# Kernel optimization log

Measured on AMD Instinct MI355X. Metric: run time of the kernel, lower is better.

The kernel has to match this reference:

```python
import jax, jax.numpy as jnp
import numpy as np

N, E, G = 50000, 600000, 256
IN_C, EMB, HID, OUT = 64, 128, 128, 36


def _glorot(key, fan_in, fan_out):
    lim = np.sqrt(6.0 / (fan_in + fan_out)).astype(np.float32)
    return jax.random.uniform(key, (fan_in, fan_out), jnp.float32, -lim, lim)


def setup_inputs() -> dict:
    key = jax.random.key(0)
    ks = jax.random.split(key, 12)
    x = jax.random.normal(ks[0], (N, IN_C), jnp.float32)
    edge_index = jax.random.randint(ks[1], (2, E), 0, N, jnp.int64)
    edge_attr = jax.random.uniform(ks[2], (E,), jnp.float32)
    # deterministic sorted batch assignment -> every graph id 0..G-1 is nonempty
    batch = ((jnp.arange(N, dtype=jnp.int64) * G) // N).astype(jnp.int64)
    rho = jax.random.uniform(ks[3], (G,), jnp.float32)
    return {
        "x": x,
        "edge_attr": edge_attr,
        "rho": rho,
        "conv0_w": _glorot(ks[4], IN_C, EMB),
        "conv0_b": jnp.zeros((EMB,), jnp.float32),
        "conv1_w": _glorot(ks[5], EMB, EMB),
        "conv1_b": jnp.zeros((EMB,), jnp.float32),
        "mlp0_w": _glorot(ks[6], 2 * EMB + 1, HID),
        "mlp0_b": jnp.zeros((HID,), jnp.float32),
        "mlp1_w": _glorot(ks[7], HID, HID),
        "mlp1_b": jnp.zeros((HID,), jnp.float32),
        "out_w": _glorot(ks[8], HID, OUT),
        "out_b": jnp.zeros((OUT,), jnp.float32),
        "edge_index": edge_index,
        "batch": batch,
    }


def _gcn_conv(h, row, col, w, W, b):
    # PyG GCNConv: self-loops already appended in (row, col, w).
    deg = jax.ops.segment_sum(w, col, num_segments=N)  # in-degree by edge weight
    dis = jnp.where(deg > 0, jax.lax.rsqrt(jnp.maximum(deg, 1e-30)), 0.0)
    norm = dis[row] * w * dis[col]                     # [E+N]
    h = h @ W                                          # [N, out]
    msg = norm[:, None] * h[row]                       # gather + scale
    return jax.ops.segment_sum(msg, col, num_segments=N) + b


def reference(x, edge_attr, rho, conv0_w, conv0_b, conv1_w, conv1_b,
              mlp0_w, mlp0_b, mlp1_w, mlp1_b, out_w, out_b,
              edge_index, batch):
    # add self-loops with weight 1
    loops = jnp.arange(N, dtype=edge_index.dtype)
    row = jnp.concatenate([edge_index[0], loops])
    col = jnp.concatenate([edge_index[1], loops])
    w = jnp.concatenate([edge_attr, jnp.ones((N,), edge_attr.dtype)])

    h = jax.nn.relu(_gcn_conv(x, row, col, w, conv0_w, conv0_b))
    h = jax.nn.relu(_gcn_conv(h, row, col, w, conv1_w, conv1_b))

    gmp = jax.ops.segment_max(h, batch, num_segments=G)             # [G, EMB]
    cnt = jax.ops.segment_sum(jnp.ones((N,), h.dtype), batch, num_segments=G)
    gap = jax.ops.segment_sum(h, batch, num_segments=G) / cnt[:, None]
    hg = jnp.concatenate([gmp, gap, rho[:, None]], axis=1)          # [G, 2*EMB+1]

    hg = jax.nn.relu(hg @ mlp0_w + mlp0_b)
    hg = jax.nn.relu(hg @ mlp1_w + mlp1_b)
    return hg @ out_w + out_b
```

## Files before the change

### kernel.cpp

```cpp
#include <hip/hip_runtime.h>
#include <hip/hip_fp16.h>
#include <math.h>

using half8 = __attribute__((ext_vector_type(8))) _Float16;
using f32x4 = __attribute__((ext_vector_type(4))) float;

#define CAP 64


__device__ __forceinline__ float wdec(unsigned int v) {
    __half h;
    *reinterpret_cast<unsigned short*>(&h) = (unsigned short)(v >> 16);
    return __half2float(h);
}

__device__ __forceinline__ unsigned int wenc(int src, float w) {
    __half h = __float2half(w);
    return (unsigned int)src |
           ((unsigned int)(*reinterpret_cast<unsigned short*>(&h)) << 16);
}

__device__ __forceinline__ float4 ld_half4(const __half* p) {
    int2 raw = *reinterpret_cast<const int2*>(p);
    __half2 a = *reinterpret_cast<__half2*>(&raw.x);
    __half2 b = *reinterpret_cast<__half2*>(&raw.y);
    return make_float4(__low2float(a), __high2float(a), __low2float(b), __high2float(b));
}

__device__ __forceinline__ void st_half4(__half* p, float4 v) {
    __half2 a = __floats2half2_rn(v.x, v.y);
    __half2 b = __floats2half2_rn(v.z, v.w);
    int2 raw;
    raw.x = *reinterpret_cast<int*>(&a);
    raw.y = *reinterpret_cast<int*>(&b);
    *reinterpret_cast<int2*>(p) = raw;
}


__global__ void k_setup(const float* __restrict__ w0, __half* __restrict__ wt0,
                        const float* __restrict__ w1, __half* __restrict__ wt1,
                        int* __restrict__ cursor, float* __restrict__ pmax,
                        float* __restrict__ psum, int n, int gch) {
    int i = blockIdx.x * blockDim.x + threadIdx.x;
    if (i < 64 * 128) {
        int k = i >> 7, c = i & 127;
        wt0[c * 64 + k] = __float2half(w0[i]);
    }
    if (i < 128 * 128) {
        int k = i >> 7, c = i & 127;
        wt1[c * 128 + k] = __float2half(w1[i]);
    }
    if (i < n) cursor[i] = 0;
    if (i < gch) { pmax[i] = 0.f; psum[i] = 0.f; }
}


__global__ void k_place(const int* __restrict__ row, const int* __restrict__ col,
                        const float* __restrict__ w, int* __restrict__ cursor,
                        unsigned int* __restrict__ slab, int e) {
    int i = blockIdx.x * blockDim.x + threadIdx.x;
    if (i < e) {
        int c = col[i];
        int s = atomicAdd(&cursor[c], 1);
        if (s < CAP) slab[(size_t)c * CAP + s] = wenc(row[i], w[i]);
    }
}

__global__ __launch_bounds__(256) void k_degscale(
    const unsigned int* __restrict__ slab, const int* __restrict__ cursor,
    const float* __restrict__ x, float* __restrict__ dis,
    __half* __restrict__ xs, int n)
{
    __shared__ float sdis[256];
    int t = threadIdx.x;
    int base = blockIdx.x * 256;
    int i = base + t;
    if (i < n) {
        int cnt = min(cursor[i], CAP);
        float s = 1.0f;
        const unsigned int* p = &slab[(size_t)i * CAP];
        int j = 0;
        for (; j + 4 <= cnt; j += 4) {
            uint4 rec = *reinterpret_cast<const uint4*>(&p[j]);
            s += wdec(rec.x) + wdec(rec.y) + wdec(rec.z) + wdec(rec.w);
        }
        for (; j < cnt; ++j) s += wdec(p[j]);
        float d = rsqrtf(s);
        dis[i] = d;
        sdis[t] = d;
    }
    __syncthreads();
#pragma unroll
    for (int it = 0; it < 16; ++it) {
        int id = it * 256 + t;
        int node_l = id >> 4;
        if (base + node_l < n) {
            float d = sdis[node_l];
            float4 v = reinterpret_cast<const float4*>(x)[(size_t)base * 16 + id];
            v.x *= d; v.y *= d; v.z *= d; v.w *= d;
            st_half4(&xs[((size_t)base * 16 + id) * 4], v);
        }
    }
}


template<int COLS, int LPN>
__global__ __launch_bounds__(256) void k_agg(
    const __half* __restrict__ hs, const unsigned int* __restrict__ slab,
    const int* __restrict__ cursor, const float* __restrict__ dis,
    __half* __restrict__ out, int n)
{
    int t = blockIdx.x * blockDim.x + threadIdx.x;
    int node = t / LPN, lane = t % LPN;
    if (node >= n) return;
    int c4 = lane * 4;
    float4 acc = ld_half4(&hs[(size_t)node * COLS + c4]);
    int cnt = min(cursor[node], CAP);
    const unsigned int* sp = &slab[(size_t)node * CAP];
    int p = 0;
    for (; p + 4 <= cnt; p += 4) {
        uint4 rec = *reinterpret_cast<const uint4*>(&sp[p]);
        float w0 = wdec(rec.x), w1 = wdec(rec.y), w2 = wdec(rec.z), w3 = wdec(rec.w);
        float4 v0 = ld_half4(&hs[(size_t)(rec.x & 0xFFFF) * COLS + c4]);
        float4 v1 = ld_half4(&hs[(size_t)(rec.y & 0xFFFF) * COLS + c4]);
        float4 v2 = ld_half4(&hs[(size_t)(rec.z & 0xFFFF) * COLS + c4]);
        float4 v3 = ld_half4(&hs[(size_t)(rec.w & 0xFFFF) * COLS + c4]);
        acc.x = fmaf(w0, v0.x, acc.x); acc.y = fmaf(w0, v0.y, acc.y);
        acc.z = fmaf(w0, v0.z, acc.z); acc.w = fmaf(w0, v0.w, acc.w);
        acc.x = fmaf(w1, v1.x, acc.x); acc.y = fmaf(w1, v1.y, acc.y);
        acc.z = fmaf(w1, v1.z, acc.z); acc.w = fmaf(w1, v1.w, acc.w);
        acc.x = fmaf(w2, v2.x, acc.x); acc.y = fmaf(w2, v2.y, acc.y);
        acc.z = fmaf(w2, v2.z, acc.z); acc.w = fmaf(w2, v2.w, acc.w);
        acc.x = fmaf(w3, v3.x, acc.x); acc.y = fmaf(w3, v3.y, acc.y);
        acc.z = fmaf(w3, v3.z, acc.z); acc.w = fmaf(w3, v3.w, acc.w);
    }
    for (; p < cnt; ++p) {
        unsigned int rec = sp[p];
        float w0 = wdec(rec);
        float4 v0 = ld_half4(&hs[(size_t)(rec & 0xFFFF) * COLS + c4]);
        acc.x = fmaf(w0, v0.x, acc.x); acc.y = fmaf(w0, v0.y, acc.y);
        acc.z = fmaf(w0, v0.z, acc.z); acc.w = fmaf(w0, v0.w, acc.w);
    }
    float d = dis[node];
    float4 o;
    o.x = d * acc.x; o.y = d * acc.y; o.z = d * acc.z; o.w = d * acc.w;
    st_half4(&out[(size_t)node * COLS + c4], o);
}


template<int K, bool SC, bool POOL>
__global__ __launch_bounds__(256) void k_gemm_mfma(
    const __half* __restrict__ A, const __half* __restrict__ wt,
    const float* __restrict__ bias, const float* __restrict__ scale,
    const int* __restrict__ batch, float* __restrict__ pmax,
    float* __restrict__ psum, __half* __restrict__ out, int n)
{
    constexpr int SA = K + 8;
    constexpr int CPR = K / 8;
    __shared__ _Float16 Al[64 * SA];
    __shared__ _Float16 Wl[128 * SA];
    const int tid = threadIdx.x;
    const int row0 = blockIdx.x * 64;

#pragma unroll
    for (int it = 0; it < (64 * CPR) / 256; ++it) {
        int id = tid + it * 256;
        int r = id / CPR, kc = id % CPR;
        int gr = row0 + r; if (gr >= n) gr = n - 1;
        int4 raw = *reinterpret_cast<const int4*>(&A[(size_t)gr * K + kc * 8]);
        *reinterpret_cast<int4*>(&Al[r * SA + kc * 8]) = raw;
    }
#pragma unroll
    for (int it = 0; it < (128 * CPR) / 256; ++it) {
        int id = tid + it * 256;
        int c = id / CPR, kc = id % CPR;
        int4 raw = *reinterpret_cast<const int4*>(&wt[(size_t)c * K + kc * 8]);
        *reinterpret_cast<int4*>(&Wl[c * SA + kc * 8]) = raw;
    }
    __syncthreads();

    const int l = tid & 63, w = tid >> 6;
    const int r = l & 15, kg = l >> 4;

    f32x4 acc[8];
#pragma unroll
    for (int ct = 0; ct < 8; ++ct) acc[ct] = (f32x4){0.f, 0.f, 0.f, 0.f};

#pragma unroll
    for (int kst = 0; kst < K / 32; ++kst) {
        half8 af = *reinterpret_cast<const half8*>(&Al[(16 * w + r) * SA + kst * 32 + kg * 8]);
#pragma unroll
        for (int ct = 0; ct < 8; ++ct) {
            half8 bf = *reinterpret_cast<const half8*>(&Wl[(16 * ct + r) * SA + kst * 32 + kg * 8]);
            acc[ct] = __builtin_amdgcn_mfma_f32_16x16x32_f16(af, bf, acc[ct], 0, 0, 0);
        }
    }

    float sc[4];
    int bq[4];
    int g0 = 0, g1 = 0;
    if constexpr (POOL) {
        g0 = batch[row0];
        g1 = batch[(row0 + 63 < n) ? row0 + 63 : n - 1];
    }
#pragma unroll
    for (int q = 0; q < 4; ++q) {
        int gr = row0 + 16 * w + kg * 4 + q;
        sc[q] = (SC && gr < n) ? scale[gr] : 1.0f;
        if constexpr (POOL) bq[q] = (gr < n) ? (batch[gr] - g0) : -1;
    }
    float pm0[8], ps0[8], pm1[8], ps1[8];
    if constexpr (POOL) {
#pragma unroll
        for (int ct = 0; ct < 8; ++ct) { pm0[ct] = 0.f; ps0[ct] = 0.f; pm1[ct] = 0.f; ps1[ct] = 0.f; }
    }
#pragma unroll
    for (int ct = 0; ct < 8; ++ct) {
        float bv = bias[16 * ct + r];
#pragma unroll
        for (int q = 0; q < 4; ++q) {
            int gr = row0 + 16 * w + kg * 4 + q;
            if (gr < n) {
                float v = fmaxf(acc[ct][q] + bv, 0.f);
                if constexpr (SC) v *= sc[q];
                out[(size_t)gr * 128 + 16 * ct + r] = __float2half(v);
                if constexpr (POOL) {
                    if (bq[q] == 0) { pm0[ct] = fmaxf(pm0[ct], v); ps0[ct] += v; }
                    else if (bq[q] == 1) { pm1[ct] = fmaxf(pm1[ct], v); ps1[ct] += v; }
                }
            }
        }
    }

    if constexpr (POOL) {
#pragma unroll
        for (int mask = 16; mask <= 32; mask <<= 1) {
#pragma unroll
            for (int ct = 0; ct < 8; ++ct) {
                pm0[ct] = fmaxf(pm0[ct], __shfl_xor(pm0[ct], mask));
                ps0[ct] += __shfl_xor(ps0[ct], mask);
                pm1[ct] = fmaxf(pm1[ct], __shfl_xor(pm1[ct], mask));
                ps1[ct] += __shfl_xor(ps1[ct], mask);
            }
        }
        __syncthreads();
        float* ldsm = reinterpret_cast<float*>(Wl);
        float* ldss = ldsm + 4 * 2 * 128;
        if (kg == 0) {
#pragma unroll
            for (int ct = 0; ct < 8; ++ct) {
                int ch = 16 * ct + r;
                ldsm[(w * 2 + 0) * 128 + ch] = pm0[ct];
                ldsm[(w * 2 + 1) * 128 + ch] = pm1[ct];
                ldss[(w * 2 + 0) * 128 + ch] = ps0[ct];
                ldss[(w * 2 + 1) * 128 + ch] = ps1[ct];
            }
        }
        __syncthreads();
        int gslot = tid >> 7, ch = tid & 127;
        bool valid = (gslot == 0) || (g1 != g0);
        if (valid) {
            float M = 0.f, S = 0.f;
#pragma unroll
            for (int ww = 0; ww < 4; ++ww) {
                M = fmaxf(M, ldsm[(ww * 2 + gslot) * 128 + ch]);
                S += ldss[(ww * 2 + gslot) * 128 + ch];
            }
            int g = g0 + gslot;
            atomicMax(reinterpret_cast<int*>(&pmax[(size_t)g * 128 + ch]), __float_as_int(M));
            atomicAdd(&psum[(size_t)g * 128 + ch], S);
        }
    }
}


__device__ __forceinline__ int lowbound(const int* __restrict__ b, int n, int key) {
    int lo = 0, hi = n;
    while (lo < hi) { int mid = (lo + hi) >> 1; if (b[mid] < key) lo = mid + 1; else hi = mid; }
    return lo;
}

__global__ __launch_bounds__(256) void k_head_mlp(
    const float* __restrict__ pmax, const float* __restrict__ psum,
    const int* __restrict__ batch, const float* __restrict__ rho,
    const float* __restrict__ w0, const float* __restrict__ b0,
    const float* __restrict__ w1, const float* __restrict__ b1,
    const float* __restrict__ w2, const float* __restrict__ b2,
    float* __restrict__ out, int n)
{
    int g = blockIdx.x;
    int tid = threadIdx.x;
    int ch = tid & 127, half = tid >> 7;
    __shared__ float hg[257];
    __shared__ float t0[128];
    __shared__ float red[2][128];
    __shared__ int scnt;
    if (tid == 0) {
        int beg = lowbound(batch, n, g);
        int end = lowbound(batch, n, g + 1);
        scnt = end - beg;
        hg[256] = rho[g];
    }
    __syncthreads();
    if (half == 0) {
        hg[ch] = pmax[(size_t)g * 128 + ch];
        hg[128 + ch] = psum[(size_t)g * 128 + ch] / (float)scnt;
    }
    __syncthreads();
    {
        float a = 0.f, b = 0.f;
        int j0 = half * 128;
        int jend = half ? 257 : 128;
        int j = j0;
        for (; j + 2 <= jend; j += 2) {
            a = fmaf(hg[j], w0[(size_t)j * 128 + ch], a);
            b = fmaf(hg[j + 1], w0[(size_t)(j + 1) * 128 + ch], b);
        }
        if (j < jend) a = fmaf(hg[j], w0[(size_t)j * 128 + ch], a);
        red[half][ch] = a + b;
        __syncthreads();
        if (half == 0) t0[ch] = fmaxf(red[0][ch] + red[1][ch] + b0[ch], 0.f);
        __syncthreads();
    }
    {
        float a = 0.f, b = 0.f;
        int j0 = half * 64;
        for (int j = j0; j < j0 + 64; j += 2) {
            a = fmaf(t0[j], w1[(size_t)j * 128 + ch], a);
            b = fmaf(t0[j + 1], w1[(size_t)(j + 1) * 128 + ch], b);
        }
        red[half][ch] = a + b;
        __syncthreads();
        if (half == 0) hg[ch] = fmaxf(red[0][ch] + red[1][ch] + b1[ch], 0.f);
        __syncthreads();
    }
    if (ch < 36) {
        float a = 0.f, b = 0.f;
        int j0 = half * 64;
        for (int j = j0; j < j0 + 64; j += 2) {
            a = fmaf(hg[j], w2[(size_t)j * 36 + ch], a);
            b = fmaf(hg[j + 1], w2[(size_t)(j + 1) * 36 + ch], b);
        }
        red[half][ch] = a + b;
    }
    __syncthreads();
    if (half == 0 && ch < 36)
        out[(size_t)g * 36 + ch] = red[0][ch] + red[1][ch] + b2[ch];
}


extern "C" void kernel_launch(void* const* d_in, const int* in_sizes, int n_in,
                              void* d_out, int out_size, void* d_ws, size_t ws_size,
                              hipStream_t stream)
{
    const float* x        = (const float*)d_in[0];
    const float* edge_attr= (const float*)d_in[1];
    const float* rho      = (const float*)d_in[2];
    const float* conv0_w  = (const float*)d_in[3];
    const float* conv0_b  = (const float*)d_in[4];
    const float* conv1_w  = (const float*)d_in[5];
    const float* conv1_b  = (const float*)d_in[6];
    const float* mlp0_w   = (const float*)d_in[7];
    const float* mlp0_b   = (const float*)d_in[8];
    const float* mlp1_w   = (const float*)d_in[9];
    const float* mlp1_b   = (const float*)d_in[10];
    const float* out_w    = (const float*)d_in[11];
    const float* out_b    = (const float*)d_in[12];
    const int*   edge_idx = (const int*)d_in[13];
    const int*   batch    = (const int*)d_in[14];

    const int N = in_sizes[0] / 64;
    const int E = in_sizes[1];
    const int G = in_sizes[2];
    const int* erow = edge_idx;
    const int* ecol = edge_idx + E;

    char* ws = (char*)d_ws;
    size_t off = 0;
    auto alloc = [&](size_t bytes) -> void* {
        off = (off + 255) & ~(size_t)255;
        void* p = ws + off;
        off += bytes;
        return p;
    };
    float*        dis    = (float*)alloc((size_t)N * 4);
    int*          cursor = (int*)  alloc((size_t)N * 4);
    unsigned int* slab   = (unsigned int*)alloc((size_t)N * CAP * 4);
    __half*       bufA   = (__half*)alloc((size_t)N * 128 * 2);
    __half*       bufB   = (__half*)alloc((size_t)N * 128 * 2);
    float*        pmax   = (float*)alloc((size_t)G * 128 * 4);
    float*        psum   = (float*)alloc((size_t)G * 128 * 4);
    __half*       wt0    = (__half*)alloc((size_t)64 * 128 * 2);
    __half*       wt1    = (__half*)alloc((size_t)128 * 128 * 2);

    dim3 b256(256);
    int gch = G * 128;
    int setup_n = N;
    if (setup_n < 128 * 128) setup_n = 128 * 128;
    if (setup_n < gch) setup_n = gch;
    k_setup<<<(setup_n + 255) / 256, b256, 0, stream>>>(conv0_w, wt0, conv1_w, wt1,
                                                       cursor, pmax, psum, N, gch);
    k_place<<<(E + 255) / 256, b256, 0, stream>>>(erow, ecol, edge_attr, cursor, slab, E);
    k_degscale<<<(N + 255) / 256, b256, 0, stream>>>(slab, cursor, x, dis, bufA, N);

    k_agg<64, 16><<<((size_t)N * 16 + 255) / 256, b256, 0, stream>>>(bufA, slab, cursor, dis, bufB, N);
    k_gemm_mfma<64, true, false><<<(N + 63) / 64, b256, 0, stream>>>(
        bufB, wt0, conv0_b, dis, nullptr, nullptr, nullptr, bufA, N);
    k_agg<128, 32><<<((size_t)N * 32 + 255) / 256, b256, 0, stream>>>(bufA, slab, cursor, dis, bufB, N);
    k_gemm_mfma<128, false, true><<<(N + 63) / 64, b256, 0, stream>>>(
        bufB, wt1, conv1_b, nullptr, batch, pmax, psum, bufA, N);

    k_head_mlp<<<G, b256, 0, stream>>>(pmax, psum, batch, rho,
                                       mlp0_w, mlp0_b, mlp1_w, mlp1_b, out_w, out_b,
                                       (float*)d_out, N);
}
```

Baseline: 157.0 us.

## Replace global-atomic CSR placement with two-pass block-bucketed partition

Edge placement no longer does one global atomic per edge into a per-node slab. Edges are first bucketed by 256-node block, with shared-memory ranking and one global atomic per bucket per CTA. A second kernel then builds each block's slab image in LDS, computes degrees from summed weights and scales x in the same pass. This reduces global atomic contention and scattered writes, at the cost of an extra intermediate buffer and pass. Slab capacity drops from 64 to 48 per node, and the fixed region size could truncate edges for skewed inputs.

```diff
diff --git a/kernel.cpp b/kernel.cpp
--- a/kernel.cpp
+++ b/kernel.cpp
@@ -5,7 +5,10 @@
 using half8 = __attribute__((ext_vector_type(8))) _Float16;
 using f32x4 = __attribute__((ext_vector_type(4))) float;
 
-#define CAP 64
+#define CAP 48
+#define NPBSH 8
+#define REG 4096
+#define BSTRIDE 16
 
 
 __device__ __forceinline__ float wdec(unsigned int v) {
@@ -39,8 +42,8 @@
 
 __global__ void k_setup(const float* __restrict__ w0, __half* __restrict__ wt0,
                         const float* __restrict__ w1, __half* __restrict__ wt1,
-                        int* __restrict__ cursor, float* __restrict__ pmax,
-                        float* __restrict__ psum, int n, int gch) {
+                        int* __restrict__ bcnt, float* __restrict__ pmax,
+                        float* __restrict__ psum, int nbp, int gch) {
     int i = blockIdx.x * blockDim.x + threadIdx.x;
     if (i < 64 * 128) {
         int k = i >> 7, c = i & 127;
@@ -50,56 +53,99 @@
         int k = i >> 7, c = i & 127;
         wt1[c * 128 + k] = __float2half(w1[i]);
     }
-    if (i < n) cursor[i] = 0;
+    if (i < nbp) bcnt[i] = 0;
     if (i < gch) { pmax[i] = 0.f; psum[i] = 0.f; }
 }
 
 
-__global__ void k_place(const int* __restrict__ row, const int* __restrict__ col,
-                        const float* __restrict__ w, int* __restrict__ cursor,
-                        unsigned int* __restrict__ slab, int e) {
-    int i = blockIdx.x * blockDim.x + threadIdx.x;
-    if (i < e) {
-        int c = col[i];
-        int s = atomicAdd(&cursor[c], 1);
-        if (s < CAP) slab[(size_t)c * CAP + s] = wenc(row[i], w[i]);
-    }
-}
-
-__global__ __launch_bounds__(256) void k_degscale(
-    const unsigned int* __restrict__ slab, const int* __restrict__ cursor,
-    const float* __restrict__ x, float* __restrict__ dis,
+__global__ __launch_bounds__(256) void k_partA(
+    const int* __restrict__ row, const int* __restrict__ col,
+    const float* __restrict__ w, int* __restrict__ bcnt,
+    uint2* __restrict__ regn, int e, int nb)
+{
+    __shared__ int lcnt[256];
+    __shared__ int lbase[256];
+    const int tid = threadIdx.x;
+    for (int b = tid; b < nb; b += 256) lcnt[b] = 0;
+    __syncthreads();
+    const int base = blockIdx.x * 2048;
+    int myb[8], myrank[8];
+#pragma unroll
+    for (int k = 0; k < 8; ++k) {
+        int i = base + k * 256 + tid;
+        if (i < e) {
+            int b = col[i] >> NPBSH;
+            myb[k] = b;
+            myrank[k] = atomicAdd(&lcnt[b], 1);
+        } else myb[k] = -1;
+    }
+    __syncthreads();
+    for (int b = tid; b < nb; b += 256) {
+        int c = lcnt[b];
+        lbase[b] = (c > 0) ? atomicAdd(&bcnt[b * BSTRIDE], c) : 0;
+    }
+    __syncthreads();
+#pragma unroll
+    for (int k = 0; k < 8; ++k) {
+        int i = base + k * 256 + tid;
+        if (myb[k] >= 0) {
+            int pos = lbase[myb[k]] + myrank[k];
+            if (pos < REG) {
+                uint2 rec;
+                rec.x = (unsigned)row[i] | (((unsigned)col[i] & 255u) << 16);
+                rec.y = __float_as_uint(w[i]);
+                regn[(size_t)myb[k] * REG + pos] = rec;
+            }
+        }
+    }
+}
+
+
+__global__ __launch_bounds__(256) void k_partB(
+    const uint2* __restrict__ regn, const int* __restrict__ bcnt,
+    const float* __restrict__ x, unsigned int* __restrict__ slab,
+    int* __restrict__ cnt_g, float* __restrict__ dis,
     __half* __restrict__ xs, int n)
 {
+    __shared__ unsigned int simg[256 * CAP];
+    __shared__ int lcnt[256];
+    __shared__ float lwsum[256];
     __shared__ float sdis[256];
-    int t = threadIdx.x;
-    int base = blockIdx.x * 256;
-    int i = base + t;
-    if (i < n) {
-        int cnt = min(cursor[i], CAP);
-        float s = 1.0f;
-        const unsigned int* p = &slab[(size_t)i * CAP];
-        int j = 0;
-        for (; j + 4 <= cnt; j += 4) {
-            uint4 rec = *reinterpret_cast<const uint4*>(&p[j]);
-            s += wdec(rec.x) + wdec(rec.y) + wdec(rec.z) + wdec(rec.w);
-        }
-        for (; j < cnt; ++j) s += wdec(p[j]);
-        float d = rsqrtf(s);
-        dis[i] = d;
-        sdis[t] = d;
-    }
-    __syncthreads();
-#pragma unroll
-    for (int it = 0; it < 16; ++it) {
-        int id = it * 256 + t;
-        int node_l = id >> 4;
-        if (base + node_l < n) {
-            float d = sdis[node_l];
-            float4 v = reinterpret_cast<const float4*>(x)[(size_t)base * 16 + id];
-            v.x *= d; v.y *= d; v.z *= d; v.w *= d;
-            st_half4(&xs[((size_t)base * 16 + id) * 4], v);
-        }
+    const int tid = threadIdx.x;
+    const int b = blockIdx.x;
+    lcnt[tid] = 0; lwsum[tid] = 0.f;
+    __syncthreads();
+    int ce = bcnt[b * BSTRIDE]; if (ce > REG) ce = REG;
+    for (int i = tid; i < ce; i += 256) {
+        uint2 rec = regn[(size_t)b * REG + i];
+        int nl = (rec.x >> 16) & 255;
+        int r = (int)(rec.x & 0xFFFFu);
+        float w = __uint_as_float(rec.y);
+        int s = atomicAdd(&lcnt[nl], 1);
+        if (s < CAP) simg[nl * CAP + s] = wenc(r, w);
+        atomicAdd(&lwsum[nl], w);
+    }
+    __syncthreads();
+    const int node0 = b << NPBSH;
+    int nodes_here = n - node0; if (nodes_here > 256) nodes_here = 256;
+    if (nodes_here <= 0) return;
+    if (tid < nodes_here) {
+        int node = node0 + tid;
+        int c = lcnt[tid]; if (c > CAP) c = CAP;
+        cnt_g[node] = c;
+        float d = rsqrtf(1.0f + lwsum[tid]);
+        dis[node] = d;
+        sdis[tid] = d;
+    }
+    __syncthreads();
+    for (int idx = tid; idx < nodes_here * CAP; idx += 256)
+        slab[(size_t)node0 * CAP + idx] = simg[idx];
+    for (int q = tid; q < nodes_here * 16; q += 256) {
+        int nl = q >> 4;
+        float d = sdis[nl];
+        float4 v = reinterpret_cast<const float4*>(x)[(size_t)node0 * 16 + q];
+        v.x *= d; v.y *= d; v.z *= d; v.w *= d;
+        st_half4(&xs[((size_t)node0 * 16 + q) * 4], v);
     }
 }
 
@@ -374,6 +420,7 @@
     const int G = in_sizes[2];
     const int* erow = edge_idx;
     const int* ecol = edge_idx + E;
+    const int NB = (N + 255) >> NPBSH;
 
     char* ws = (char*)d_ws;
     size_t off = 0;
@@ -384,7 +431,9 @@
         return p;
     };
     float*        dis    = (float*)alloc((size_t)N * 4);
-    int*          cursor = (int*)  alloc((size_t)N * 4);
+    int*          cnt_g  = (int*)  alloc((size_t)N * 4);
+    int*          bcnt   = (int*)  alloc((size_t)NB * BSTRIDE * 4);
+    uint2*        regn   = (uint2*)alloc((size_t)NB * REG * 8);
     unsigned int* slab   = (unsigned int*)alloc((size_t)N * CAP * 4);
     __half*       bufA   = (__half*)alloc((size_t)N * 128 * 2);
     __half*       bufB   = (__half*)alloc((size_t)N * 128 * 2);
@@ -395,18 +444,19 @@
 
     dim3 b256(256);
     int gch = G * 128;
-    int setup_n = N;
-    if (setup_n < 128 * 128) setup_n = 128 * 128;
+    int nbp = NB * BSTRIDE;
+    int setup_n = 128 * 128;
+    if (setup_n < nbp) setup_n = nbp;
     if (setup_n < gch) setup_n = gch;
     k_setup<<<(setup_n + 255) / 256, b256, 0, stream>>>(conv0_w, wt0, conv1_w, wt1,
-                                                       cursor, pmax, psum, N, gch);
-    k_place<<<(E + 255) / 256, b256, 0, stream>>>(erow, ecol, edge_attr, cursor, slab, E);
-    k_degscale<<<(N + 255) / 256, b256, 0, stream>>>(slab, cursor, x, dis, bufA, N);
-
-    k_agg<64, 16><<<((size_t)N * 16 + 255) / 256, b256, 0, stream>>>(bufA, slab, cursor, dis, bufB, N);
+                                                       bcnt, pmax, psum, nbp, gch);
+    k_partA<<<(E + 2047) / 2048, b256, 0, stream>>>(erow, ecol, edge_attr, bcnt, regn, E, NB);
+    k_partB<<<NB, b256, 0, stream>>>(regn, bcnt, x, slab, cnt_g, dis, bufA, N);
+
+    k_agg<64, 16><<<((size_t)N * 16 + 255) / 256, b256, 0, stream>>>(bufA, slab, cnt_g, dis, bufB, N);
     k_gemm_mfma<64, true, false><<<(N + 63) / 64, b256, 0, stream>>>(
         bufB, wt0, conv0_b, dis, nullptr, nullptr, nullptr, bufA, N);
-    k_agg<128, 32><<<((size_t)N * 32 + 255) / 256, b256, 0, stream>>>(bufA, slab, cursor, dis, bufB, N);
+    k_agg<128, 32><<<((size_t)N * 32 + 255) / 256, b256, 0, stream>>>(bufA, slab, cnt_g, dis, bufB, N);
     k_gemm_mfma<128, false, true><<<(N + 63) / 64, b256, 0, stream>>>(
         bufB, wt1, conv1_b, nullptr, batch, pmax, psum, bufA, N);
 
```

New measurement: 144.1 us. -8.2%, faster.
